# Performance work log

Hardware: AMD Instinct MI355X
Metric: run time of the kernel (lower is better)

## Reference

```python
import jax, jax.numpy as jnp
import numpy as np

B, N, D, U = 128, 1024, 16, 128


def setup_inputs() -> dict:
    key = jax.random.key(0)
    ks = jax.random.split(key, 12)
    # get_normalized_adj: D^{-1/2} (A + I) D^{-1/2} on a sparse random graph
    A = (jax.random.uniform(ks[0], (N, N)) < 0.01).astype(jnp.float32)
    A = A + jnp.eye(N, dtype=jnp.float32)
    dinv = 1.0 / jnp.sqrt(A.sum(axis=1))
    support = dinv[:, None] * A * dinv[None, :]
    s = 0.05
    return {
        "x": jax.random.normal(ks[1], (2, B, N, D), jnp.float32),
        "hx": jax.random.normal(ks[2], (B, N * U), jnp.float32),
        "delta": jax.random.normal(ks[3], (B, N, D), jnp.float32),
        "support": support,
        "kernel_r": jax.random.normal(ks[4], (D + U, 2 * U), jnp.float32) * jnp.sqrt(2.0 / (D + U)),
        "kernel_c": jax.random.normal(ks[5], (D + U, U), jnp.float32) * jnp.sqrt(2.0 / (D + U)),
        "w_out": jax.random.normal(ks[6], (U + D, D), jnp.float32) * s,
        "b_out": jax.random.normal(ks[7], (D,), jnp.float32) * s,
        "w_basis": jax.random.normal(ks[8], (D, D), jnp.float32) * s,
        "b_basis": jax.random.normal(ks[9], (D,), jnp.float32) * s,
        "lam": jax.random.normal(ks[10], (1,), jnp.float32),
    }


def reference(x, hx, delta, support, kernel_r, kernel_c, w_out, b_out, w_basis, b_basis, lam):
    y_basis, y_res = x[0], x[1]                       # (B, N, D) each
    # speculative delta (add=True branch)
    delta_value = jax.nn.relu(y_res @ w_basis + b_basis)
    p_t = jax.nn.sigmoid(y_res + 0.5 * jnp.sqrt(jnp.abs(delta + 1e-9)))
    new_delta = lam * (2.0 * p_t - 1.0) * delta_value  # (B, N, D)

    hx3 = hx.reshape(B, N, U)

    def gconv(inp, state, kernel):
        # inp (B,N,D), state (B,N,U); diffusion_step == 1 Chebyshev pass
        xs = jnp.concatenate([inp, state], axis=-1)      # (B, N, D+U)
        xs = jnp.einsum('ij,bjl->bil', support, xs)      # diffusion over nodes
        return xs @ kernel                               # (B, N, out)

    value = jax.nn.sigmoid(gconv(y_basis, hx3, kernel_r))  # (B, N, 2U)
    r, u = value[..., :U], value[..., U:]
    c = jnp.tanh(gconv(y_basis, r * hx3, kernel_c))        # (B, N, U)

    u_flat = u.reshape(B, N * U)
    c_flat = c.reshape(B, N * U)
    new_state = hx * u_flat + c_flat * (1.0 - u_flat)      # (B, N*U)

    concat = jnp.concatenate([new_state.reshape(B, N, U), y_basis], axis=-1)
    o = concat @ w_out + b_out + new_delta                 # (B, N, D)
    return (o, new_state, new_delta)
```

## Files before the change

kernel.cpp:

```cpp
#include <hip/hip_runtime.h>
#include <cstdint>

#define B_ 128
#define N_ 1024
#define D_ 16
#define U_ 128
#define M_ (B_*N_)
#define K_ 144
#define KP 192
#define CAP 48

typedef unsigned short u16;
typedef unsigned int   u32;
typedef __attribute__((ext_vector_type(8))) short bf16x8;
typedef __attribute__((ext_vector_type(4))) float f32x4;
typedef __attribute__((ext_vector_type(2))) __fp16 h2v;

__device__ __forceinline__ float bf2f(u16 h){ return __uint_as_float(((u32)h) << 16); }
__device__ __forceinline__ u16 f2bf(float f){
    u32 u = __float_as_uint(f);
    return (u16)((u + 0x7FFFu + ((u >> 16) & 1u)) >> 16);
}
__device__ __forceinline__ u16 f2h(float f){
    __fp16 h = (__fp16)f; u16 s; __builtin_memcpy(&s, &h, 2); return s;
}
__device__ __forceinline__ float h2f_lo(u32 u){
    u16 s = (u16)(u & 0xFFFFu); __fp16 h; __builtin_memcpy(&h, &s, 2); return (float)h;
}
__device__ __forceinline__ float h2f_hi(u32 u){
    u16 s = (u16)(u >> 16); __fp16 h; __builtin_memcpy(&h, &s, 2); return (float)h;
}
__device__ __forceinline__ u32 pkrtz(float a, float b){
    h2v r = __builtin_amdgcn_cvt_pkrtz(a, b);
    u32 v; __builtin_memcpy(&v, &r, 4); return v;
}
__device__ __forceinline__ float sig_(float x){ return 1.0f / (1.0f + __expf(-x)); }

#if __has_builtin(__builtin_amdgcn_fdot2)
__device__ __forceinline__ float dot2_(u32 a, u32 b, float c){
    h2v av, bv; __builtin_memcpy(&av, &a, 4); __builtin_memcpy(&bv, &b, 4);
    return __builtin_amdgcn_fdot2(av, bv, c, false);
}
#else
__device__ __forceinline__ float dot2_(u32 a, u32 b, float c){
    return fmaf(h2f_hi(a), h2f_hi(b), fmaf(h2f_lo(a), h2f_lo(b), c));
}
#endif

__global__ void k_ellprep(const float* __restrict__ sup,
                          const float* __restrict__ kr, const float* __restrict__ kc,
                          float* __restrict__ vals, int* __restrict__ cols,
                          int* __restrict__ nnz, u32* __restrict__ packed,
                          u16* __restrict__ wr_t, u16* __restrict__ wc_t)
{
    if (blockIdx.x >= 256){
        int t = (blockIdx.x - 256) * 256 + threadIdx.x;
        if (t < 256*KP){
            int col = t / KP, k = t % KP;
            wr_t[t] = f2bf(k < K_ ? kr[k*256 + col] : 0.0f);
        } else {
            int q = t - 256*KP;
            int col = q / KP, k = q % KP;
            wc_t[q] = f2bf(k < K_ ? kc[k*128 + col] : 0.0f);
        }
        return;
    }
    int wid  = (blockIdx.x * blockDim.x + threadIdx.x) >> 6;
    int lane = threadIdx.x & 63;
    if (wid >= N_) return;
    const float* row = sup + (size_t)wid * N_;
    int base = 0;
    for (int step = 0; step < N_/64; ++step){
        int j = step*64 + lane;
        float v = row[j];
        unsigned long long m = __ballot(v != 0.0f);
        int pos = base + __popcll(m & ((1ull << lane) - 1ull));
        if (v != 0.0f && pos < CAP){
            vals[wid*CAP + pos] = v; cols[wid*CAP + pos] = j;
            if (pos < 16) packed[wid*16 + pos] = (u32)f2h(v) | ((u32)j << 16);
        }
        base += __popcll(m);
    }
    int cnt = base < CAP ? base : CAP;
    for (int p = cnt + lane; p < CAP; p += 64){
        vals[wid*CAP + p] = 0.0f;
        cols[wid*CAP + p] = 0;
        if (p < 16) packed[wid*16 + p] = 0;
    }
    if (lane == 0) nnz[wid] = (cnt + 3) & ~3;
}


#define GQD(E0, E1)                                                            \
    {   u32 wp = __builtin_amdgcn_perm((E1), (E0), 0x05040100u);               \
        int c0 = (int)((E0) >> 16), c1 = (int)((E1) >> 16);                    \
        uint2 hh0 = *(const uint2*)(s16 + c0*16 + cq*4);                       \
        uint2 hh1 = *(const uint2*)(s16 + c1*16 + cq*4);                       \
        u32 pa0 = __builtin_amdgcn_perm(hh1.x, hh0.x, 0x05040100u);            \
        u32 pa1 = __builtin_amdgcn_perm(hh1.x, hh0.x, 0x07060302u);            \
        u32 pa2 = __builtin_amdgcn_perm(hh1.y, hh0.y, 0x05040100u);            \
        u32 pa3 = __builtin_amdgcn_perm(hh1.y, hh0.y, 0x07060302u);            \
        acc.x = dot2_(wp, pa0, acc.x); acc.y = dot2_(wp, pa1, acc.y);          \
        acc.z = dot2_(wp, pa2, acc.z); acc.w = dot2_(wp, pa3, acc.w); }

#define GQH(JJ, WW)                                                            \
    {   uint2 hh = *(const uint2*)(s16 + (int)(JJ)*16 + cq*4);                 \
        acc.x = fmaf((WW), h2f_lo(hh.x), acc.x);                               \
        acc.y = fmaf((WW), h2f_hi(hh.x), acc.y);                               \
        acc.z = fmaf((WW), h2f_lo(hh.y), acc.z);                               \
        acc.w = fmaf((WW), h2f_hi(hh.y), acc.w); }

#define GB_G(T0)                                                               \
    {   float4 wvt = *(const float4*)(vt + (T0));                              \
        int4   jvt = *(const int4*)(ct + (T0));                                \
        GQH(jvt.x, wvt.x); GQH(jvt.y, wvt.y);                                  \
        GQH(jvt.z, wvt.z); GQH(jvt.w, wvt.w); }

#define GATHER_PACKED(STORE_EXPR)                                              \
    for (int p = tid; p < 4096; p += 512){                                     \
        int node = p >> 2, cq = p & 3;                                         \
        const u32* ep = packed + node*16;                                      \
        uint4 e0 = *(const uint4*)(ep);                                        \
        uint4 e1 = *(const uint4*)(ep + 4);                                    \
        uint4 e2 = *(const uint4*)(ep + 8);                                    \
        uint4 e3 = *(const uint4*)(ep + 12);                                   \
        int c = nnz[node];                                                     \
        float4 acc = make_float4(0.f,0.f,0.f,0.f);                             \
        GQD(e0.x, e0.y) GQD(e0.z, e0.w)                                        \
        GQD(e1.x, e1.y) GQD(e1.z, e1.w)                                        \
        GQD(e2.x, e2.y) GQD(e2.z, e2.w)                                        \
        GQD(e3.x, e3.y) GQD(e3.z, e3.w)                                        \
        if (c > 16){                                                           \
            const float* vt = vals + node*CAP;                                 \
            const int*   ct = cols + node*CAP;                                 \
            for (int t0 = 16; t0 < c; t0 += 4) GB_G(t0)                        \
        }                                                                      \
        size_t m = (size_t)(b<<10) + node;                                     \
        ushort4 pv; pv.x = f2bf(acc.x); pv.y = f2bf(acc.y);                    \
        pv.z = f2bf(acc.z); pv.w = f2bf(acc.w);                                \
        STORE_EXPR;                                                            \
    }

#define PACKH8(PK, VA, VB)                                                     \
    uint4 PK; PK.x = pkrtz((VA).x, (VA).y); PK.y = pkrtz((VA).z, (VA).w);      \
    PK.z = pkrtz((VB).x, (VB).y); PK.w = pkrtz((VB).z, (VB).w);

__global__ __launch_bounds__(512, 8) void k_spmm1(
        const float* __restrict__ x, const float* __restrict__ hx,
        const u32* __restrict__ packed,
        const float* __restrict__ vals, const int* __restrict__ cols,
        const int* __restrict__ nnz, u16* __restrict__ agg)
{
    __shared__ u16 s16[1024*16];
    const int chunk = blockIdx.x;
    const int b     = blockIdx.y;
    const int tid   = threadIdx.x;
    const int cb    = chunk * 16;

    for (int q = tid; q < 2048; q += 512){
        int row = q >> 1, part = q & 1;
        const float* src = (chunk == 0)
            ? &x[((size_t)((b<<10)+row))*16 + part*8]
            : &hx[((size_t)((b<<10)+row))*128 + (cb-16) + part*8];
        float4 va = *(const float4*)src;
        float4 vb = *(const float4*)(src + 4);
        PACKH8(pk, va, vb)
        *(uint4*)(s16 + row*16 + part*8) = pk;
    }
    __syncthreads();

    GATHER_PACKED(*(ushort4*)&agg[m*KP + cb + cq*4] = pv)
}

__global__ __launch_bounds__(512, 8) void k_spmm2(
        const u16* __restrict__ value, const float* __restrict__ hx,
        const u32* __restrict__ packed,
        const float* __restrict__ vals, const int* __restrict__ cols,
        const int* __restrict__ nnz, u16* __restrict__ agg)
{
    __shared__ u16 s16[1024*16];
    const int chunk = blockIdx.x;
    const int b     = blockIdx.y;
    const int tid   = threadIdx.x;
    const int cb    = chunk * 16;

    for (int q = tid; q < 2048; q += 512){
        int row = q >> 1, part = q & 1;
        size_t nb = (size_t)((b<<10)+row);
        int hxcol = cb + part*8;
        float4 h0 = *(const float4*)&hx[nb*128 + hxcol];
        float4 h1 = *(const float4*)&hx[nb*128 + hxcol + 4];
        ushort4 r0 = *(const ushort4*)&value[nb*256 + hxcol];
        ushort4 r1 = *(const ushort4*)&value[nb*256 + hxcol + 4];
        float4 va = make_float4(bf2f(r0.x)*h0.x, bf2f(r0.y)*h0.y,
                                bf2f(r0.z)*h0.z, bf2f(r0.w)*h0.w);
        float4 vb = make_float4(bf2f(r1.x)*h1.x, bf2f(r1.y)*h1.y,
                                bf2f(r1.z)*h1.z, bf2f(r1.w)*h1.w);
        PACKH8(pk, va, vb)
        *(uint4*)(s16 + row*16 + part*8) = pk;
    }
    __syncthreads();

    GATHER_PACKED(*(ushort4*)&agg[m*KP + D_ + cb + cq*4] = pv)
}

__global__ __launch_bounds__(256) void k_gemm1(const u16* __restrict__ agg,
        const u16* __restrict__ wt, u16* __restrict__ value)
{
    __shared__ u16 a_s[128*72];
    __shared__ u16 w_s[128*72];
    const int rb = blockIdx.x * 128, cb = blockIdx.y * 128;
    const int tid = threadIdx.x;
    const int wid = tid >> 6, lane = tid & 63;
    const int wr = (wid >> 1) * 64, wc = (wid & 1) * 64;
    const int lrow = lane & 15, lk = (lane >> 4) * 8;
    f32x4 acc[4][4] = {};
    for (int kb = 0; kb < KP; kb += 64){
        __syncthreads();
        #pragma unroll
        for (int i2 = 0; i2 < 4; ++i2){
            int q = tid + i2*256;
            int r_ = q >> 3, sl = q & 7;
            uint4 v = {0,0,0,0};
            if (kb + sl*8 < K_)
                v = *(const uint4*)(agg + (size_t)(rb+r_)*KP + kb + sl*8);
            *(uint4*)(a_s + r_*72 + sl*8) = v;
        }
        #pragma unroll
        for (int i2 = 0; i2 < 4; ++i2){
            int q = tid + i2*256;
            int r_ = q >> 3, sl = q & 7;
            uint4 v = *(const uint4*)(wt + (size_t)(cb+r_)*KP + kb + sl*8);
            *(uint4*)(w_s + r_*72 + sl*8) = v;
        }
        __syncthreads();
        #pragma unroll
        for (int ks = 0; ks < 2; ++ks){
            bf16x8 af[4], bfv[4];
            #pragma unroll
            for (int f = 0; f < 4; ++f){
                af[f]  = *(const bf16x8*)(a_s + (wr + f*16 + lrow)*72 + ks*32 + lk);
                bfv[f] = *(const bf16x8*)(w_s + (wc + f*16 + lrow)*72 + ks*32 + lk);
            }
            #pragma unroll
            for (int fr = 0; fr < 4; ++fr)
                #pragma unroll
                for (int fc = 0; fc < 4; ++fc)
                    acc[fr][fc] = __builtin_amdgcn_mfma_f32_16x16x32_bf16(
                        af[fr], bfv[fc], acc[fr][fc], 0, 0, 0);
        }
    }
    const int rg = (lane >> 4) * 4;
    #pragma unroll
    for (int fr = 0; fr < 4; ++fr)
        #pragma unroll
        for (int fc = 0; fc < 4; ++fc)
            #pragma unroll
            for (int j = 0; j < 4; ++j){
                int row = rb + wr + fr*16 + rg + j;
                int col = cb + wc + fc*16 + lrow;
                value[(size_t)row*256 + col] = f2bf(sig_(acc[fr][fc][j]));
            }
}

__global__ __launch_bounds__(256) void k_gemm2(const u16* __restrict__ agg,
        const u16* __restrict__ wt, const float* __restrict__ hx,
        const u16* value, float* ns_out)
{
    __shared__ u16 a_s[128*72];
    __shared__ u16 w_s[128*72];
    const int rb = blockIdx.x * 128;
    const int tid = threadIdx.x;
    const int wid = tid >> 6, lane = tid & 63;
    const int wr = (wid >> 1) * 64, wc = (wid & 1) * 64;
    const int lrow = lane & 15, lk = (lane >> 4) * 8;
    f32x4 acc[4][4] = {};
    for (int kb = 0; kb < KP; kb += 64){
        __syncthreads();
        #pragma unroll
        for (int i2 = 0; i2 < 4; ++i2){
            int q = tid + i2*256;
            int r_ = q >> 3, sl = q & 7;
            uint4 v = {0,0,0,0};
            if (kb + sl*8 < K_)
                v = *(const uint4*)(agg + (size_t)(rb+r_)*KP + kb + sl*8);
            *(uint4*)(a_s + r_*72 + sl*8) = v;
        }
        #pragma unroll
        for (int i2 = 0; i2 < 4; ++i2){
            int q = tid + i2*256;
            int r_ = q >> 3, sl = q & 7;
            uint4 v = *(const uint4*)(wt + (size_t)r_*KP + kb + sl*8);
            *(uint4*)(w_s + r_*72 + sl*8) = v;
        }
        __syncthreads();
        #pragma unroll
        for (int ks = 0; ks < 2; ++ks){
            bf16x8 af[4], bfv[4];
            #pragma unroll
            for (int f = 0; f < 4; ++f){
                af[f]  = *(const bf16x8*)(a_s + (wr + f*16 + lrow)*72 + ks*32 + lk);
                bfv[f] = *(const bf16x8*)(w_s + (wc + f*16 + lrow)*72 + ks*32 + lk);
            }
            #pragma unroll
            for (int fr = 0; fr < 4; ++fr)
                #pragma unroll
                for (int fc = 0; fc < 4; ++fc)
                    acc[fr][fc] = __builtin_amdgcn_mfma_f32_16x16x32_bf16(
                        af[fr], bfv[fc], acc[fr][fc], 0, 0, 0);
        }
    }
    const int rg = (lane >> 4) * 4;
    float ov[4][4][4];
    #pragma unroll
    for (int fr = 0; fr < 4; ++fr)
        #pragma unroll
        for (int fc = 0; fc < 4; ++fc)
            #pragma unroll
            for (int j = 0; j < 4; ++j){
                int row = rb + wr + fr*16 + rg + j;
                int col = wc + fc*16 + lrow;
                float u = bf2f(value[(size_t)row*256 + 128 + col]);
                float h = hx[(size_t)row*128 + col];
                float c = tanhf(acc[fr][fc][j]);
                ov[fr][fc][j] = h*u + c*(1.0f - u);
            }
    __syncthreads();
    #pragma unroll
    for (int fr = 0; fr < 4; ++fr)
        #pragma unroll
        for (int fc = 0; fc < 4; ++fc)
            #pragma unroll
            for (int j = 0; j < 4; ++j){
                int row = rb + wr + fr*16 + rg + j;
                int col = wc + fc*16 + lrow;
                ns_out[(size_t)row*128 + col] = ov[fr][fc][j];
            }
}

__global__ __launch_bounds__(256) void k_out(const float* __restrict__ ns,
        const float* __restrict__ x, const float* __restrict__ delta,
        const float* __restrict__ wo, const float* __restrict__ bo,
        const float* __restrict__ wb, const float* __restrict__ bb,
        const float* __restrict__ lam,
        float* __restrict__ o, float* __restrict__ nd_out)
{
    __shared__ float ns_s[64][132];
    __shared__ float yb_s[64][20];
    __shared__ float yr_s[64][20];
    __shared__ float w_s[144][16];
    __shared__ float wb_s[16][16];
    __shared__ float bo_s[16], bb_s[16];
    int rowbase = blockIdx.x * 64;
    int tid = threadIdx.x;
    const float* yr = x + (size_t)M_ * D_;
    #pragma unroll
    for (int jj = 0; jj < 8; ++jj){
        int q = tid + 256*jj;
        int row = q >> 5, c4 = (q & 31) * 4;
        *(float4*)&ns_s[row][c4] = *(const float4*)&ns[(size_t)(rowbase + row)*U_ + c4];
    }
    {
        int row = tid >> 2, c4 = (tid & 3) * 4;
        *(float4*)&yb_s[row][c4] = *(const float4*)&x[(size_t)(rowbase + row)*D_ + c4];
        *(float4*)&yr_s[row][c4] = *(const float4*)&yr[(size_t)(rowbase + row)*D_ + c4];
    }
    #pragma unroll
    for (int jj = 0; jj < 3; ++jj){
        int q = tid + 256*jj;
        if (q < 576){ int k = q >> 2, d4 = (q & 3) * 4;
            *(float4*)&w_s[k][d4] = *(const float4*)&wo[k*D_ + d4]; }
    }
    wb_s[tid >> 4][tid & 15] = wb[tid];
    if (tid < 16){ bo_s[tid] = bo[tid]; bb_s[tid] = bb[tid]; }
    __syncthreads();
    int row = tid >> 2, d0 = (tid & 3) * 4;
    float4 acc = make_float4(0.f,0.f,0.f,0.f);
    for (int k = 0; k < U_; ++k){
        float cs = ns_s[row][k];
        float4 w = *(const float4*)&w_s[k][d0];
        acc.x = fmaf(cs, w.x, acc.x); acc.y = fmaf(cs, w.y, acc.y);
        acc.z = fmaf(cs, w.z, acc.z); acc.w = fmaf(cs, w.w, acc.w);
    }
    #pragma unroll
    for (int k = 0; k < D_; ++k){
        float cs = yb_s[row][k];
        float4 w = *(const float4*)&w_s[U_ + k][d0];
        acc.x = fmaf(cs, w.x, acc.x); acc.y = fmaf(cs, w.y, acc.y);
        acc.z = fmaf(cs, w.z, acc.z); acc.w = fmaf(cs, w.w, acc.w);
    }
    float4 dacc = make_float4(bb_s[d0], bb_s[d0+1], bb_s[d0+2], bb_s[d0+3]);
    #pragma unroll
    for (int k = 0; k < D_; ++k){
        float yv = yr_s[row][k];
        float4 w = *(const float4*)&wb_s[k][d0];
        dacc.x = fmaf(yv, w.x, dacc.x); dacc.y = fmaf(yv, w.y, dacc.y);
        dacc.z = fmaf(yv, w.z, dacc.z); dacc.w = fmaf(yv, w.w, dacc.w);
    }
    size_t off = (size_t)(rowbase + row)*D_ + d0;
    float4 dl = *(const float4*)&delta[off];
    float lm = lam[0];
    float nd4[4];
    float yv4[4] = {yr_s[row][d0], yr_s[row][d0+1], yr_s[row][d0+2], yr_s[row][d0+3]};
    float dv4[4] = {fmaxf(dacc.x,0.f), fmaxf(dacc.y,0.f), fmaxf(dacc.z,0.f), fmaxf(dacc.w,0.f)};
    float dl4[4] = {dl.x, dl.y, dl.z, dl.w};
    #pragma unroll
    for (int j = 0; j < 4; ++j){
        float pt = sig_(yv4[j] + 0.5f * sqrtf(fabsf(dl4[j] + 1e-9f)));
        nd4[j] = lm * (2.0f * pt - 1.0f) * dv4[j];
    }
    float4 bov = *(const float4*)&bo_s[d0];
    float4 ov = make_float4(acc.x + bov.x + nd4[0], acc.y + bov.y + nd4[1],
                            acc.z + bov.z + nd4[2], acc.w + bov.w + nd4[3]);
    *(float4*)&nd_out[off] = make_float4(nd4[0], nd4[1], nd4[2], nd4[3]);
    *(float4*)&o[off] = ov;
}

extern "C" void kernel_launch(void* const* d_in, const int* in_sizes, int n_in,
                              void* d_out, int out_size, void* d_ws, size_t ws_size,
                              hipStream_t stream)
{
    const float* x        = (const float*)d_in[0];
    const float* hx       = (const float*)d_in[1];
    const float* delta    = (const float*)d_in[2];
    const float* support  = (const float*)d_in[3];
    const float* kernel_r = (const float*)d_in[4];
    const float* kernel_c = (const float*)d_in[5];
    const float* w_out    = (const float*)d_in[6];
    const float* b_out    = (const float*)d_in[7];
    const float* w_basis  = (const float*)d_in[8];
    const float* b_basis  = (const float*)d_in[9];
    const float* lam      = (const float*)d_in[10];

    float* out = (float*)d_out;
    float* o   = out;
    float* ns  = out + 2097152;
    float* nd  = out + 18874368;
    u16*   value = (u16*)ns;

    char* ws = (char*)d_ws;
    float* ell_vals = (float*)ws;
    int*   ell_cols = (int*)(ws + 196608);
    int*   ell_nnz  = (int*)(ws + 393216);
    u32*   ell_pk   = (u32*)(ws + 397312);
    u16*   agg      = (u16*)(ws + (1 << 20));
    u16*   wr_t     = (u16*)(ws + (1 << 20) + (size_t)M_*KP*2);
    u16*   wc_t     = wr_t + 256*KP;

    k_ellprep<<<544, 256, 0, stream>>>(support, kernel_r, kernel_c,
                                       ell_vals, ell_cols, ell_nnz, ell_pk,
                                       wr_t, wc_t);
    k_spmm1<<<dim3(9,128), 512, 0, stream>>>(x, hx, ell_pk,
                                             ell_vals, ell_cols, ell_nnz, agg);
    k_gemm1<<<dim3(M_/128, 2), 256, 0, stream>>>(agg, wr_t, value);
    k_spmm2<<<dim3(8,128), 512, 0, stream>>>(value, hx, ell_pk,
                                             ell_vals, ell_cols, ell_nnz, agg);
    k_gemm2<<<M_/128, 256, 0, stream>>>(agg, wc_t, hx, value, ns);
    k_out  <<<M_/64, 256, 0, stream>>>(ns, x, delta, w_out, b_out,
                                       w_basis, b_basis, lam, o, nd);
}
```

Measured before the change: 228.7 us.

## Widen SpMM feature chunks from 16 to 32 columns per block

The two sparse aggregation kernels now process 32 feature columns per block instead of 16. Each thread gathers 8 columns, so the ELL index/weight loads and permutes are amortised over twice the work, and each thread issues 16-byte stores. This halves the number of blocks and the re-reads of the sparse structure. In exchange, shared memory per block doubles, launch bounds drop to 4 blocks per CU, and the first kernel's last chunk is padded and partly masked.

```diff
diff --git a/kernel.cpp b/kernel.cpp
--- a/kernel.cpp
+++ b/kernel.cpp
@@ -91,32 +91,32 @@
 }
 
 
-#define GQD(E0, E1)                                                            \
+#define GQD8(E0, E1)                                                           \
     {   u32 wp = __builtin_amdgcn_perm((E1), (E0), 0x05040100u);               \
         int c0 = (int)((E0) >> 16), c1 = (int)((E1) >> 16);                    \
-        uint2 hh0 = *(const uint2*)(s16 + c0*16 + cq*4);                       \
-        uint2 hh1 = *(const uint2*)(s16 + c1*16 + cq*4);                       \
-        u32 pa0 = __builtin_amdgcn_perm(hh1.x, hh0.x, 0x05040100u);            \
-        u32 pa1 = __builtin_amdgcn_perm(hh1.x, hh0.x, 0x07060302u);            \
-        u32 pa2 = __builtin_amdgcn_perm(hh1.y, hh0.y, 0x05040100u);            \
-        u32 pa3 = __builtin_amdgcn_perm(hh1.y, hh0.y, 0x07060302u);            \
-        acc.x = dot2_(wp, pa0, acc.x); acc.y = dot2_(wp, pa1, acc.y);          \
-        acc.z = dot2_(wp, pa2, acc.z); acc.w = dot2_(wp, pa3, acc.w); }
-
-#define GQH(JJ, WW)                                                            \
-    {   uint2 hh = *(const uint2*)(s16 + (int)(JJ)*16 + cq*4);                 \
-        acc.x = fmaf((WW), h2f_lo(hh.x), acc.x);                               \
-        acc.y = fmaf((WW), h2f_hi(hh.x), acc.y);                               \
-        acc.z = fmaf((WW), h2f_lo(hh.y), acc.z);                               \
-        acc.w = fmaf((WW), h2f_hi(hh.y), acc.w); }
-
-#define GB_G(T0)                                                               \
-    {   float4 wvt = *(const float4*)(vt + (T0));                              \
-        int4   jvt = *(const int4*)(ct + (T0));                                \
-        GQH(jvt.x, wvt.x); GQH(jvt.y, wvt.y);                                  \
-        GQH(jvt.z, wvt.z); GQH(jvt.w, wvt.w); }
-
-#define GATHER_PACKED(STORE_EXPR)                                              \
+        uint4 h0 = *(const uint4*)(s16 + c0*32 + cq*8);                        \
+        uint4 h1 = *(const uint4*)(s16 + c1*32 + cq*8);                        \
+        u32 p0 = __builtin_amdgcn_perm(h1.x, h0.x, 0x05040100u);               \
+        u32 p1 = __builtin_amdgcn_perm(h1.x, h0.x, 0x07060302u);               \
+        u32 p2 = __builtin_amdgcn_perm(h1.y, h0.y, 0x05040100u);               \
+        u32 p3 = __builtin_amdgcn_perm(h1.y, h0.y, 0x07060302u);               \
+        u32 p4 = __builtin_amdgcn_perm(h1.z, h0.z, 0x05040100u);               \
+        u32 p5 = __builtin_amdgcn_perm(h1.z, h0.z, 0x07060302u);               \
+        u32 p6 = __builtin_amdgcn_perm(h1.w, h0.w, 0x05040100u);               \
+        u32 p7 = __builtin_amdgcn_perm(h1.w, h0.w, 0x07060302u);               \
+        a0 = dot2_(wp, p0, a0); a1 = dot2_(wp, p1, a1);                        \
+        a2 = dot2_(wp, p2, a2); a3 = dot2_(wp, p3, a3);                        \
+        a4 = dot2_(wp, p4, a4); a5 = dot2_(wp, p5, a5);                        \
+        a6 = dot2_(wp, p6, a6); a7 = dot2_(wp, p7, a7); }
+
+#define GQH8(JJ, WW)                                                           \
+    {   uint4 hh = *(const uint4*)(s16 + (int)(JJ)*32 + cq*8);                 \
+        a0 = fmaf((WW), h2f_lo(hh.x), a0); a1 = fmaf((WW), h2f_hi(hh.x), a1);  \
+        a2 = fmaf((WW), h2f_lo(hh.y), a2); a3 = fmaf((WW), h2f_hi(hh.y), a3);  \
+        a4 = fmaf((WW), h2f_lo(hh.z), a4); a5 = fmaf((WW), h2f_hi(hh.z), a5);  \
+        a6 = fmaf((WW), h2f_lo(hh.w), a6); a7 = fmaf((WW), h2f_hi(hh.w), a7); }
+
+#define GATHER32(STORE_EXPR)                                                   \
     for (int p = tid; p < 4096; p += 512){                                     \
         int node = p >> 2, cq = p & 3;                                         \
         const u32* ep = packed + node*16;                                      \
@@ -125,83 +125,93 @@
         uint4 e2 = *(const uint4*)(ep + 8);                                    \
         uint4 e3 = *(const uint4*)(ep + 12);                                   \
         int c = nnz[node];                                                     \
-        float4 acc = make_float4(0.f,0.f,0.f,0.f);                             \
-        GQD(e0.x, e0.y) GQD(e0.z, e0.w)                                        \
-        GQD(e1.x, e1.y) GQD(e1.z, e1.w)                                        \
-        GQD(e2.x, e2.y) GQD(e2.z, e2.w)                                        \
-        GQD(e3.x, e3.y) GQD(e3.z, e3.w)                                        \
+        float a0=0.f,a1=0.f,a2=0.f,a3=0.f,a4=0.f,a5=0.f,a6=0.f,a7=0.f;         \
+        GQD8(e0.x, e0.y) GQD8(e0.z, e0.w)                                      \
+        GQD8(e1.x, e1.y) GQD8(e1.z, e1.w)                                      \
+        GQD8(e2.x, e2.y) GQD8(e2.z, e2.w)                                      \
+        GQD8(e3.x, e3.y) GQD8(e3.z, e3.w)                                      \
         if (c > 16){                                                           \
             const float* vt = vals + node*CAP;                                 \
             const int*   ct = cols + node*CAP;                                 \
-            for (int t0 = 16; t0 < c; t0 += 4) GB_G(t0)                        \
+            for (int t0 = 16; t0 < c; t0 += 4){                                \
+                float4 wvt = *(const float4*)(vt + t0);                        \
+                int4   jvt = *(const int4*)(ct + t0);                          \
+                GQH8(jvt.x, wvt.x) GQH8(jvt.y, wvt.y)                          \
+                GQH8(jvt.z, wvt.z) GQH8(jvt.w, wvt.w)                          \
+            }                                                                  \
         }                                                                      \
         size_t m = (size_t)(b<<10) + node;                                     \
-        ushort4 pv; pv.x = f2bf(acc.x); pv.y = f2bf(acc.y);                    \
-        pv.z = f2bf(acc.z); pv.w = f2bf(acc.w);                                \
+        uint4 pv; pv.x = (u32)f2bf(a0) | ((u32)f2bf(a1) << 16);                \
+        pv.y = (u32)f2bf(a2) | ((u32)f2bf(a3) << 16);                          \
+        pv.z = (u32)f2bf(a4) | ((u32)f2bf(a5) << 16);                          \
+        pv.w = (u32)f2bf(a6) | ((u32)f2bf(a7) << 16);                          \
         STORE_EXPR;                                                            \
     }
 
-#define PACKH8(PK, VA, VB)                                                     \
-    uint4 PK; PK.x = pkrtz((VA).x, (VA).y); PK.y = pkrtz((VA).z, (VA).w);      \
-    PK.z = pkrtz((VB).x, (VB).y); PK.w = pkrtz((VB).z, (VB).w);
-
-__global__ __launch_bounds__(512, 8) void k_spmm1(
+__global__ __launch_bounds__(512, 4) void k_spmm1(
         const float* __restrict__ x, const float* __restrict__ hx,
         const u32* __restrict__ packed,
         const float* __restrict__ vals, const int* __restrict__ cols,
         const int* __restrict__ nnz, u16* __restrict__ agg)
 {
-    __shared__ u16 s16[1024*16];
+    __shared__ u16 s16[1024*32];
     const int chunk = blockIdx.x;
     const int b     = blockIdx.y;
     const int tid   = threadIdx.x;
-    const int cb    = chunk * 16;
-
-    for (int q = tid; q < 2048; q += 512){
-        int row = q >> 1, part = q & 1;
-        const float* src = (chunk == 0)
-            ? &x[((size_t)((b<<10)+row))*16 + part*8]
-            : &hx[((size_t)((b<<10)+row))*128 + (cb-16) + part*8];
-        float4 va = *(const float4*)src;
-        float4 vb = *(const float4*)(src + 4);
-        PACKH8(pk, va, vb)
-        *(uint4*)(s16 + row*16 + part*8) = pk;
+    const int cb    = chunk * 32;
+
+    for (int q = tid; q < 4096; q += 512){
+        int row = q >> 2, part = q & 3;
+        int xscol = cb + part*8;
+        uint4 pk = {0,0,0,0};
+        if (xscol < 16){
+            const float* src = &x[((size_t)((b<<10)+row))*16 + xscol];
+            float4 va = *(const float4*)src, vb = *(const float4*)(src + 4);
+            pk.x = pkrtz(va.x, va.y); pk.y = pkrtz(va.z, va.w);
+            pk.z = pkrtz(vb.x, vb.y); pk.w = pkrtz(vb.z, vb.w);
+        } else if (xscol < K_){
+            const float* src = &hx[((size_t)((b<<10)+row))*128 + (xscol-16)];
+            float4 va = *(const float4*)src, vb = *(const float4*)(src + 4);
+            pk.x = pkrtz(va.x, va.y); pk.y = pkrtz(va.z, va.w);
+            pk.z = pkrtz(vb.x, vb.y); pk.w = pkrtz(vb.z, vb.w);
+        }
+        *(uint4*)(s16 + row*32 + part*8) = pk;
     }
     __syncthreads();
 
-    GATHER_PACKED(*(ushort4*)&agg[m*KP + cb + cq*4] = pv)
-}
-
-__global__ __launch_bounds__(512, 8) void k_spmm2(
+    GATHER32(if (cb + cq*8 < K_) *(uint4*)&agg[m*KP + cb + cq*8] = pv)
+}
+
+__global__ __launch_bounds__(512, 4) void k_spmm2(
         const u16* __restrict__ value, const float* __restrict__ hx,
         const u32* __restrict__ packed,
         const float* __restrict__ vals, const int* __restrict__ cols,
         const int* __restrict__ nnz, u16* __restrict__ agg)
 {
-    __shared__ u16 s16[1024*16];
+    __shared__ u16 s16[1024*32];
     const int chunk = blockIdx.x;
     const int b     = blockIdx.y;
     const int tid   = threadIdx.x;
-    const int cb    = chunk * 16;
-
-    for (int q = tid; q < 2048; q += 512){
-        int row = q >> 1, part = q & 1;
+    const int cb    = chunk * 32;
+
+    for (int q = tid; q < 4096; q += 512){
+        int row = q >> 2, part = q & 3;
         size_t nb = (size_t)((b<<10)+row);
         int hxcol = cb + part*8;
         float4 h0 = *(const float4*)&hx[nb*128 + hxcol];
         float4 h1 = *(const float4*)&hx[nb*128 + hxcol + 4];
         ushort4 r0 = *(const ushort4*)&value[nb*256 + hxcol];
         ushort4 r1 = *(const ushort4*)&value[nb*256 + hxcol + 4];
-        float4 va = make_float4(bf2f(r0.x)*h0.x, bf2f(r0.y)*h0.y,
-                                bf2f(r0.z)*h0.z, bf2f(r0.w)*h0.w);
-        float4 vb = make_float4(bf2f(r1.x)*h1.x, bf2f(r1.y)*h1.y,
-                                bf2f(r1.z)*h1.z, bf2f(r1.w)*h1.w);
-        PACKH8(pk, va, vb)
-        *(uint4*)(s16 + row*16 + part*8) = pk;
+        uint4 pk;
+        pk.x = pkrtz(bf2f(r0.x)*h0.x, bf2f(r0.y)*h0.y);
+        pk.y = pkrtz(bf2f(r0.z)*h0.z, bf2f(r0.w)*h0.w);
+        pk.z = pkrtz(bf2f(r1.x)*h1.x, bf2f(r1.y)*h1.y);
+        pk.w = pkrtz(bf2f(r1.z)*h1.z, bf2f(r1.w)*h1.w);
+        *(uint4*)(s16 + row*32 + part*8) = pk;
     }
     __syncthreads();
 
-    GATHER_PACKED(*(ushort4*)&agg[m*KP + D_ + cb + cq*4] = pv)
+    GATHER32(*(uint4*)&agg[m*KP + D_ + cb + cq*8] = pv)
 }
 
 __global__ __launch_bounds__(256) void k_gemm1(const u16* __restrict__ agg,
@@ -450,10 +460,10 @@
     k_ellprep<<<544, 256, 0, stream>>>(support, kernel_r, kernel_c,
                                        ell_vals, ell_cols, ell_nnz, ell_pk,
                                        wr_t, wc_t);
-    k_spmm1<<<dim3(9,128), 512, 0, stream>>>(x, hx, ell_pk,
+    k_spmm1<<<dim3(5,128), 512, 0, stream>>>(x, hx, ell_pk,
                                              ell_vals, ell_cols, ell_nnz, agg);
     k_gemm1<<<dim3(M_/128, 2), 256, 0, stream>>>(agg, wr_t, value);
-    k_spmm2<<<dim3(8,128), 512, 0, stream>>>(value, hx, ell_pk,
+    k_spmm2<<<dim3(4,128), 512, 0, stream>>>(value, hx, ell_pk,
                                              ell_vals, ell_cols, ell_nnz, agg);
     k_gemm2<<<M_/128, 256, 0, stream>>>(agg, wc_t, hx, value, ns);
     k_out  <<<M_/64, 256, 0, stream>>>(ns, x, delta, w_out, b_out,
```

Result: faster. 214.1 us (-6.4%).
